# Kernel optimization log

Hardware: AMD Instinct MI355X
Metric: run time of the kernel (lower is better)

The kernel has to match this reference:

```python
import jax, jax.numpy as jnp
import numpy as np
import math

B, N, D = 64, 128, 128          # graphs, nodes per graph, d_model
D_STATE = 2                     # Mamba default d_state
D_CONV = 4                      # Mamba default conv kernel
DT_RANK = math.ceil(D / 16)     # 8
CUTOFF = 10.0
N_GAUSS = 50                    # GaussianSmearing(0, 10, 50)
EPS_RMS = 1e-5


def setup_inputs() -> dict:
    key = jax.random.key(0)
    ks = jax.random.split(key, 12)
    s = 0.05
    inp = {}
    inp['x'] = jax.random.normal(ks[0], (B * N, D), jnp.float32)
    inp['pos'] = jax.random.normal(ks[1], (B * N, 3), jnp.float32) * 5.0
    inp['map_idx'] = jax.random.randint(ks[2], (B * N,), 0, 16)
    inp['batch'] = jnp.repeat(jnp.arange(B), N)
    # RMSNorm
    inp['norm_w'] = jnp.ones((D,), jnp.float32)
    # simple message-passing gnn (stand-in for injected gnn module)
    inp['gnn_w1'] = jax.random.normal(ks[3], (D, D), jnp.float32) * s
    inp['gnn_b1'] = jnp.zeros((D,), jnp.float32)
    inp['gnn_w2'] = jax.random.normal(ks[4], (D, D), jnp.float32) * s
    inp['gnn_b2'] = jnp.zeros((D,), jnp.float32)
    # Linear(50, 1) on Gaussian-smeared edge distances
    inp['lin_w'] = jax.random.normal(ks[5], (N_GAUSS, 1), jnp.float32) * s
    inp['lin_b'] = jnp.zeros((1,), jnp.float32)
    # MambaBlock params (stored [in, out])
    inp['in_proj_w'] = jax.random.normal(ks[6], (D, 2 * D), jnp.float32) * s
    inp['conv_w'] = jax.random.normal(ks[7], (D, D_CONV), jnp.float32) * s
    inp['conv_b'] = jnp.zeros((D,), jnp.float32)
    inp['x_proj_w'] = jax.random.normal(ks[8], (D, DT_RANK + 2 * D_STATE), jnp.float32) * s
    inp['dt_proj_w'] = jax.random.normal(ks[9], (DT_RANK, D), jnp.float32) * s
    inp['dt_proj_b'] = jnp.zeros((D,), jnp.float32)
    inp['A_log'] = jnp.log(jnp.tile(jnp.arange(1, D_STATE + 1, dtype=jnp.float32), (D, 1)))
    inp['D_param'] = jnp.ones((D,), jnp.float32)
    inp['out_proj_w'] = jax.random.normal(ks[10], (D, D), jnp.float32) * s
    return inp


def _rmsnorm(x, w):
    return x * jax.lax.rsqrt(jnp.mean(x * x, axis=-1, keepdims=True) + EPS_RMS) * w


def _mamba(x_t, adj, in_proj_w, conv_w, conv_b, x_proj_w, dt_proj_w, dt_proj_b,
           A_log, D_param, out_proj_w):
    # x_t: [N, D] node sequence for one graph; adj: [N, N] dense edge-value matrix
    L = x_t.shape[0]
    A = -jnp.exp(A_log)                                   # [D, S]
    xr = x_t @ in_proj_w                                  # [L, 2D]
    xm, res = xr[:, :D], xr[:, D:]
    # causal depthwise conv1d (padding d_conv-1, truncated to L)
    xp = jnp.pad(xm, ((D_CONV - 1, 0), (0, 0)))
    xc = conv_b + sum(xp[j:j + L] * conv_w[:, j] for j in range(D_CONV))
    xc = jax.nn.silu(xc)                                  # [L, D]
    dbl = xc @ x_proj_w                                   # [L, dt_rank + 2S]
    delta = dbl[:, :DT_RANK]
    Bm = dbl[:, DT_RANK:DT_RANK + D_STATE]                # [L, S]
    Cm = dbl[:, DT_RANK + D_STATE:]                       # [L, S]
    delta = jax.nn.softplus(delta @ dt_proj_w + dt_proj_b)  # [L, D]
    # temp_adj_padded: ones [D, D] with adjacency slice in top-left
    m = min(L, D)
    adj_pad = jnp.ones((D, D), dtype=adj.dtype).at[:m, :m].set(adj[:m, :m])
    delta_p = delta @ adj_pad                             # [L, D]
    dA = jnp.exp(delta_p[:, :, None] * A[None])           # [L, D, S]
    dBu = delta_p[:, :, None] * Bm[:, None, :] * xc[:, :, None]

    def step(h, t):
        dA_t, dBu_t, C_t = t
        h = dA_t * h + dBu_t                              # [D, S]
        return h, h @ C_t                                 # [D]

    _, ys = jax.lax.scan(step, jnp.zeros((D, D_STATE), x_t.dtype), (dA, dBu, Cm))
    y = ys + xc * D_param
    y = y * jax.nn.silu(res)
    out = y @ out_proj_w
    return jnp.where(jnp.isfinite(out), out, 0.0)


def reference(x, pos, map_idx, batch, norm_w, gnn_w1, gnn_b1, gnn_w2, gnn_b2,
              lin_w, lin_b, in_proj_w, conv_w, conv_b, x_proj_w, dt_proj_w,
              dt_proj_b, A_log, D_param, out_proj_w):
    x1 = _rmsnorm(x, norm_w)                              # [B*N, D]
    xg = x1.reshape(B, N, D)
    pg = pos.reshape(B, N, 3)
    # per-graph radius graph (dense): dist + edge mask
    diff = pg[:, :, None, :] - pg[:, None, :, :]          # [B, N, N, 3]
    d2 = jnp.sum(diff * diff, axis=-1)
    eye = jnp.eye(N, dtype=bool)[None]
    dist = jnp.sqrt(jnp.where(eye, 1.0, d2))              # safe sqrt on diag
    edge_mask = (~eye) & (dist < CUTOFF)                  # [B, N, N]
    em = edge_mask.astype(x1.dtype)
    # simple message-passing gnn: mean-aggregate relu(Wx) over radius neighbors
    h = jax.nn.relu(xg @ gnn_w1 + gnn_b1)
    deg = jnp.clip(jnp.sum(em, axis=-1, keepdims=True), 1.0, None)
    agg = jnp.einsum('bij,bjd->bid', em, h) / deg
    x2 = agg @ gnn_w2 + gnn_b2                            # [B, N, D]
    # GaussianSmearing(0, 10, 50) + Linear(50, 1) -> dense edge-value matrix
    offsets = jnp.linspace(0.0, 10.0, N_GAUSS)
    coeff = -0.5 / (offsets[1] - offsets[0]) ** 2
    smear = jnp.exp(coeff * (dist[..., None] - offsets) ** 2)  # [B, N, N, 50]
    d_dense = smear @ lin_w[:, 0] + lin_b[0]
    adj = jnp.where(edge_mask, d_dense, 0.0)              # sparse-to-dense
    # Mamba mixer over each graph's node sequence
    mix = jax.vmap(lambda xt, a: _mamba(xt, a, in_proj_w, conv_w, conv_b,
                                        x_proj_w, dt_proj_w, dt_proj_b,
                                        A_log, D_param, out_proj_w))
    x3 = mix(x2, adj).reshape(B * N, D)
    output = x3 + x1
    return (output, pos, map_idx)
```

## Files before the change

### kernel.cpp

```cpp
#include <hip/hip_runtime.h>
#include <math.h>

#define B_ 64
#define N_ 128
#define D_ 128
#define BN_ 8192
#define NG_ 50
#define CUTOFF_ 10.0f

typedef __attribute__((ext_vector_type(8))) short short8v;
typedef __attribute__((ext_vector_type(4))) float f32x4;
#define MFMA16 __builtin_amdgcn_mfma_f32_16x16x32_bf16

__device__ __forceinline__ float bf2f(unsigned short h) {
    return __builtin_bit_cast(float, ((unsigned int)h) << 16);
}
__device__ __forceinline__ unsigned short f2bf(float f) {
    unsigned int u = __builtin_bit_cast(unsigned int, f);
    return (unsigned short)((u + 0x7FFFu + ((u >> 16) & 1u)) >> 16);
}
__device__ __forceinline__ void splitbf(float x, unsigned short& h, unsigned short& l) {
    h = f2bf(x);
    l = f2bf(x - bf2f(h));
}
__device__ __forceinline__ void gl_lds(const void* g, void* l) {
    __builtin_amdgcn_global_load_lds(
        (const __attribute__((address_space(1))) void*)g,
        (__attribute__((address_space(3))) void*)l, 16, 0, 0);
}

__global__ __launch_bounds__(256) void setup_k(
        const float* __restrict__ x, const float* __restrict__ norm_w,
        const float* __restrict__ pos, const int* __restrict__ mi,
        const float* __restrict__ lin_w, const float* __restrict__ lin_b,
        const float* __restrict__ w1, const float* __restrict__ w2,
        const float* __restrict__ b2, const float* __restrict__ in_proj,
        const float* __restrict__ xpw, const float* __restrict__ dtw,
        const float* __restrict__ out_proj,
        unsigned short* __restrict__ w1Th, unsigned short* __restrict__ w1Tl,
        unsigned short* __restrict__ WdTh, unsigned short* __restrict__ WdTl,
        unsigned short* __restrict__ opTh, unsigned short* __restrict__ opTl,
        unsigned short* __restrict__ WfTh, unsigned short* __restrict__ WfTl,
        float* __restrict__ bfv,
        float* __restrict__ x1f, unsigned short* __restrict__ x1h,
        unsigned short* __restrict__ x1l,
        unsigned short* __restrict__ adjh, unsigned short* __restrict__ adjl,
        unsigned short* __restrict__ emh, float* __restrict__ rdeg,
        float* __restrict__ out) {
    int blk = blockIdx.x, t = threadIdx.x;
    if (blk < 513) {
        if (blk < 128) {
            if (t < 128) {
                unsigned short h, l;
                splitbf(w1[blk * 128 + t], h, l);
                w1Th[t * 128 + blk] = h; w1Tl[t * 128 + blk] = l;
            }
        } else if (blk < 256) {
            int m = blk - 128;
            if (t < 128) {
                float s = 0.0f;
                #pragma unroll
                for (int r = 0; r < 8; r++) s = fmaf(xpw[m * 12 + r], dtw[r * 128 + t], s);
                unsigned short h, l; splitbf(s, h, l);
                WdTh[t * 128 + m] = h; WdTl[t * 128 + m] = l;
            }
        } else if (blk < 384) {
            int k = blk - 256;
            if (t < 128) {
                unsigned short h, l;
                splitbf(out_proj[k * 128 + t], h, l);
                opTh[t * 128 + k] = h; opTl[t * 128 + k] = l;
            }
        } else if (blk < 512) {
            int k = blk - 384;
            float s = 0.0f;
            #pragma unroll 8
            for (int j = 0; j < 128; j++) s = fmaf(w2[k * 128 + j], in_proj[j * 256 + t], s);
            unsigned short h, l; splitbf(s, h, l);
            WfTh[t * 128 + k] = h; WfTl[t * 128 + k] = l;
        } else {
            float s = 0.0f;
            #pragma unroll 8
            for (int j = 0; j < 128; j++) s = fmaf(b2[j], in_proj[j * 256 + t], s);
            bfv[t] = s;
        }
    } else if (blk < 642) {
        int idx = (blk - 513) * 256 + t;
        if (idx < BN_ * 3) out[(size_t)BN_ * D_ + idx] = pos[idx];
        if (idx < BN_) out[(size_t)BN_ * D_ + BN_ * 3 + idx] = (float)mi[idx];
    } else if (blk < 2690) {
        int rblk = blk - 642;
        int wv = t >> 6, ln = t & 63;
        int row = rblk * 4 + wv;
        const float2* xr = reinterpret_cast<const float2*>(x) + (size_t)row * 64;
        float2 v = xr[ln];
        float s = fmaf(v.x, v.x, v.y * v.y);
        #pragma unroll
        for (int o = 32; o > 0; o >>= 1) s += __shfl_down(s, o, 64);
        float tot = __shfl(s, 0, 64);
        float r = rsqrtf(tot * (1.0f / D_) + 1e-5f);
        float2 wv2 = reinterpret_cast<const float2*>(norm_w)[ln];
        float o0 = v.x * r * wv2.x, o1 = v.y * r * wv2.y;
        reinterpret_cast<float2*>(x1f)[(size_t)row * 64 + ln] = make_float2(o0, o1);
        unsigned short h0, l0, h1, l1;
        splitbf(o0, h0, l0); splitbf(o1, h1, l1);
        reinterpret_cast<ushort2*>(x1h)[(size_t)row * 64 + ln] = make_ushort2(h0, h1);
        reinterpret_cast<ushort2*>(x1l)[(size_t)row * 64 + ln] = make_ushort2(l0, l1);
    } else {
        __shared__ float px[N_], py[N_], pz[N_];
        __shared__ float lw[NG_];
        __shared__ int degs[8];
        int ablk = blk - 2690;
        int bx = ablk & 15, b = ablk >> 4;
        if (t < N_) {
            const float* p = pos + (size_t)(b * N_ + t) * 3;
            px[t] = p[0]; py[t] = p[1]; pz[t] = p[2];
        } else if (t - N_ < NG_) {
            lw[t - N_] = lin_w[t - N_];
        }
        if (t >= 248) degs[t - 248] = 0;
        __syncthreads();
        float linb = lin_b[0];
        int j = t & 127;
        int il = t >> 7;
        const float DEL = 10.0f / 49.0f;
        const float COEFF = -0.5f / (DEL * DEL);
        #pragma unroll
        for (int p = 0; p < 4; p++) {
            int i = bx * 8 + p * 2 + il;
            float dx = px[i] - px[j], dy = py[i] - py[j], dz = pz[i] - pz[j];
            float d2 = dx * dx + dy * dy + dz * dz;
            float dist = (i == j) ? 1.0f : sqrtf(d2);
            bool edge = (i != j) && (dist < CUTOFF_);
            float val = 0.0f;
            if (edge) {
                int g0 = (int)ceilf((dist - 1.75f) / DEL); if (g0 < 0) g0 = 0;
                int g1 = (int)floorf((dist + 1.75f) / DEL); if (g1 > NG_ - 1) g1 = NG_ - 1;
                float dm = dist - (float)g0 * DEL;
                float tg = expf(COEFF * dm * dm);
                float ug = expf(COEFF * DEL * (DEL - 2.0f * dm));
                float s = linb;
                for (int g = g0; g <= g1; g++) {
                    s = fmaf(lw[g], tg, s);
                    tg *= ug;
                    ug *= 0.36787944117144233f;
                }
                val = s;
            }
            size_t idx = ((size_t)b * N_ + i) * N_ + j;
            unsigned short h, l; splitbf(val, h, l);
            adjh[idx] = h; adjl[idx] = l;
            emh[idx] = edge ? 0x3F80 : 0;
            unsigned long long msk = __ballot(edge);
            if ((t & 63) == 0) atomicAdd(&degs[p * 2 + il], __popcll(msk));
        }
        __syncthreads();
        if (t < 8) {
            int dg = degs[t];
            rdeg[(size_t)b * N_ + bx * 8 + t] = 1.0f / (float)(dg > 0 ? dg : 1);
        }
    }
}

#define AHOFF 0
#define ALOFF 8192
#define BHOFF 16384
#define BLOFF 32768
template <int EPI, bool ALO>
__global__ __launch_bounds__(256, 3) void mgemm_k(
        const unsigned short* __restrict__ Ah, const unsigned short* __restrict__ Al,
        const unsigned short* __restrict__ BTh, const unsigned short* __restrict__ BTl,
        const float* __restrict__ bias, const float* __restrict__ AUX,
        float* __restrict__ Cf, unsigned short* __restrict__ Ch,
        unsigned short* __restrict__ Cl, int cstride, int wbs) {
    extern __shared__ char sm[];
    int tid = threadIdx.x;
    int row_base = blockIdx.x * 32;
    int col_base = blockIdx.y * 64;

    const unsigned short* pBh = BTh;
    const unsigned short* pBl = BTl;
    if (wbs) {
        size_t bo = (size_t)(row_base >> 7) * (size_t)wbs;
        pBh += bo; pBl += bo;
    }

    #pragma unroll
    for (int i = 0; i < 2; i++) {
        int s = tid + i * 256;
        int row = s >> 4, inner = s & 15;
        int gb = (inner * 16) ^ ((row & 7) << 4);
        size_t gsrc = (size_t)(row_base + row) * 256 + gb;
        gl_lds((const char*)Ah + gsrc, sm + AHOFF + s * 16);
        if (ALO) gl_lds((const char*)Al + gsrc, sm + ALOFF + s * 16);
    }
    #pragma unroll
    for (int i = 0; i < 4; i++) {
        int s = tid + i * 256;
        int n = s >> 4, inner = s & 15;
        int gb = (inner * 16) ^ ((n & 7) << 4);
        size_t gsrc = (size_t)(col_base + n) * 256 + gb;
        gl_lds((const char*)pBh + gsrc, sm + BHOFF + s * 16);
        gl_lds((const char*)pBl + gsrc, sm + BLOFF + s * 16);
    }
    __syncthreads();

    int w = tid >> 6, l = tid & 63;
    int rlow = l & 15, kb_lane = (l >> 4) * 16;
    int nB = w * 16 + rlow;
    int nswz = (nB & 7) << 4;
    f32x4 acc[2] = {{0.f, 0.f, 0.f, 0.f}, {0.f, 0.f, 0.f, 0.f}};
    #pragma unroll
    for (int kb = 0; kb < 4; kb++) {
        int kbyte = kb * 64 + kb_lane;
        short8v bh = *(const short8v*)(sm + BHOFF + nB * 256 + (kbyte ^ nswz));
        short8v bl = *(const short8v*)(sm + BLOFF + nB * 256 + (kbyte ^ nswz));
        #pragma unroll
        for (int rf = 0; rf < 2; rf++) {
            int ra = rf * 16 + rlow;
            int aswz = (ra & 7) << 4;
            short8v ah = *(const short8v*)(sm + AHOFF + ra * 256 + (kbyte ^ aswz));
            acc[rf] = MFMA16(ah, bh, acc[rf], 0, 0, 0);
            acc[rf] = MFMA16(ah, bl, acc[rf], 0, 0, 0);
            if (ALO) {
                short8v al_ = *(const short8v*)(sm + ALOFF + ra * 256 + (kbyte ^ aswz));
                acc[rf] = MFMA16(al_, bh, acc[rf], 0, 0, 0);
            }
        }
    }

    int colg = col_base + w * 16 + rlow;
    #pragma unroll
    for (int rf = 0; rf < 2; rf++) {
        int row0 = row_base + rf * 16 + (l >> 4) * 4;
        if (EPI == 1) {
            float b_ = bias[colg];
            unsigned short hh[4], ll[4];
            #pragma unroll
            for (int q = 0; q < 4; q++) {
                float t = fmaxf(acc[rf][q] + b_, 0.0f);
                splitbf(t, hh[q], ll[q]);
            }
            size_t bb = (size_t)(row0 >> 7) * 16384 + (size_t)colg * 128 + (row0 & 127);
            *reinterpret_cast<ushort4*>(Ch + bb) = make_ushort4(hh[0], hh[1], hh[2], hh[3]);
            *reinterpret_cast<ushort4*>(Cl + bb) = make_ushort4(ll[0], ll[1], ll[2], ll[3]);
        } else {
            #pragma unroll
            for (int q = 0; q < 4; q++) {
                int row = row0 + q;
                float t = acc[rf][q];
                if (EPI == 2) {
                    t *= AUX[row];
                    unsigned short h, lo; splitbf(t, h, lo);
                    Ch[(size_t)row * 128 + colg] = h;
                    Cl[(size_t)row * 128 + colg] = lo;
                }
                if (EPI == 5) {
                    t = isfinite(t) ? t : 0.0f;
                    t += AUX[(size_t)row * 128 + colg];
                    Cf[(size_t)row * cstride + colg] = t;
                }
            }
        }
    }
}

__device__ __forceinline__ void st128(char* dst, const char* g, int tid) {
    #pragma unroll
    for (int i = 0; i < 4; i++) {
        int s = tid + i * 512;
        int row = s >> 4, inner = s & 15;
        gl_lds(g + row * 256 + ((inner * 16) ^ ((row & 7) << 4)), dst + s * 16);
    }
}
__device__ __forceinline__ void stA48(char* dst, const char* g, int r0, int tid) {
    #pragma unroll
    for (int i = 0; i < 2; i++) {
        int s = tid + i * 512;
        if (s < 768) {
            int lr = s >> 4, inner = s & 15;
            int srow = r0 - 16 + lr; if (srow < 0) srow = 0;
            gl_lds(g + srow * 256 + ((inner * 16) ^ ((lr & 7) << 4)), dst + s * 16);
        }
    }
}
template <int NRF>
__device__ __forceinline__ void fpass(const char* sm, int ah, int al, int bh, int bl,
                                      int w, int l, f32x4 (&acc)[NRF]) {
    int rlow = l & 15, khi = (l >> 4) * 16;
    int nB = w * 16 + rlow;
    int nkey = (nB & 7) << 4;
    #pragma unroll
    for (int kb = 0; kb < 4; kb++) {
        int kbyte = kb * 64 + khi;
        short8v bhv = *(const short8v*)(sm + bh + nB * 256 + (kbyte ^ nkey));
        short8v blv = *(const short8v*)(sm + bl + nB * 256 + (kbyte ^ nkey));
        #pragma unroll
        for (int rf = 0; rf < NRF; rf++) {
            int ra = rf * 16 + rlow;
            int ao = ra * 256 + (kbyte ^ ((ra & 7) << 4));
            short8v ahv = *(const short8v*)(sm + ah + ao);
            short8v alv = *(const short8v*)(sm + al + ao);
            acc[rf] = MFMA16(ahv, bhv, acc[rf], 0, 0, 0);
            acc[rf] = MFMA16(ahv, blv, acc[rf], 0, 0, 0);
            acc[rf] = MFMA16(alv, bhv, acc[rf], 0, 0, 0);
        }
    }
}

__global__ __launch_bounds__(512, 2) void fused_k(
        const unsigned short* __restrict__ aggh, const unsigned short* __restrict__ aggl,
        const unsigned short* __restrict__ WfTh, const unsigned short* __restrict__ WfTl,
        const float* __restrict__ bfv,
        const float* __restrict__ conv_w, const float* __restrict__ conv_b,
        const float* __restrict__ xpw,
        const unsigned short* __restrict__ WdTh, const unsigned short* __restrict__ WdTl,
        const float* __restrict__ dtb,
        const unsigned short* __restrict__ adjh, const unsigned short* __restrict__ adjl,
        float* __restrict__ resT, float* __restrict__ xcT,
        float* __restrict__ bcT, float* __restrict__ dpT) {
    __shared__ __align__(16) char sm[163840];
    const int AH = 0, AL = 12288, XM = 24576, BH = 49152, BL = 81920,
              XCH = 114688, XCL = 122880, DH = 131072, DL = 139264, XCF = 147456;
    int blk = blockIdx.x, tid = threadIdx.x;
    int b = blk >> 2, r0 = (blk & 3) * 32;
    int w = tid >> 6, l = tid & 63;
    int rlow = l & 15, qrow = (l >> 4) * 4;

    stA48(sm + AH, (const char*)aggh + (size_t)b * 32768, r0, tid);
    stA48(sm + AL, (const char*)aggl + (size_t)b * 32768, r0, tid);
    st128(sm + BH, (const char*)WfTh, tid);
    st128(sm + BL, (const char*)WfTl, tid);
    __syncthreads();

    f32x4 acc[3] = {{0.f,0.f,0.f,0.f},{0.f,0.f,0.f,0.f},{0.f,0.f,0.f,0.f}};
    fpass<3>(sm, AH, AL, BH, BL, w, l, acc);
    __syncthreads();
    st128(sm + BH, (const char*)WfTh + 32768, tid);
    st128(sm + BL, (const char*)WfTl + 32768, tid);
    {
        int colg = w * 16 + rlow;
        float bb = bfv[colg];
        #pragma unroll
        for (int rf = 0; rf < 3; rf++) {
            #pragma unroll
            for (int q = 0; q < 4; q++) {
                int lr = rf * 16 + qrow + q;
                *(float*)(sm + XM + lr * 512 + ((colg * 4) ^ ((lr & 7) << 4))) =
                    acc[rf][q] + bb;
            }
        }
    }
    __syncthreads();

    f32x4 acc2[3] = {{0.f,0.f,0.f,0.f},{0.f,0.f,0.f,0.f},{0.f,0.f,0.f,0.f}};
    fpass<3>(sm, AH, AL, BH, BL, w, l, acc2);
    {
        int colg = w * 16 + rlow;
        float bb = bfv[128 + colg];
        #pragma unroll
        for (int rf = 1; rf < 3; rf++) {
            int lr0 = rf * 16 + qrow;
            int tt = r0 + lr0 - 16;
            float v[4];
            #pragma unroll
            for (int q = 0; q < 4; q++) {
                float rs = acc2[rf][q] + bb;
                v[q] = rs / (1.0f + expf(-rs));
            }
            *reinterpret_cast<float4*>(resT + ((size_t)b * 128 + colg) * 128 + tt) =
                make_float4(v[0], v[1], v[2], v[3]);
        }
    }
    __syncthreads();

    st128(sm + BH, (const char*)WdTh, tid);
    st128(sm + BL, (const char*)WdTl, tid);
    {
        int ot = tid >> 4, dg = tid & 15;
        float pc0 = 0, pc1 = 0, pc2 = 0, pc3 = 0;
        #pragma unroll
        for (int k = 0; k < 8; k++) {
            int d = dg * 8 + k;
            float accv = conv_b[d];
            #pragma unroll
            for (int jj = 0; jj < 4; jj++) {
                int tt = r0 + ot + jj - 3;
                if (tt >= 0) {
                    int lr = ot + jj - 3 + 16;
                    float xv = *(const float*)(sm + XM + lr * 512 +
                                               ((d * 4) ^ ((lr & 7) << 4)));
                    accv = fmaf(xv, conv_w[d * 4 + jj], accv);
                }
            }
            float xc = accv / (1.0f + expf(-accv));
            unsigned short hh, ll; splitbf(xc, hh, ll);
            int pb = ot * 256 + ((d * 2) ^ ((ot & 7) << 4));
            *(unsigned short*)(sm + XCH + pb) = hh;
            *(unsigned short*)(sm + XCL + pb) = ll;
            *(float*)(sm + XCF + ot * 512 + ((d * 4) ^ ((ot & 7) << 4))) = xc;
            float4 xw = *(const float4*)(xpw + d * 12 + 8);
            pc0 = fmaf(xc, xw.x, pc0); pc1 = fmaf(xc, xw.y, pc1);
            pc2 = fmaf(xc, xw.z, pc2); pc3 = fmaf(xc, xw.w, pc3);
        }
        #pragma unroll
        for (int m = 1; m < 16; m <<= 1) {
            pc0 += __shfl_xor(pc0, m, 64);
            pc1 += __shfl_xor(pc1, m, 64);
            pc2 += __shfl_xor(pc2, m, 64);
            pc3 += __shfl_xor(pc3, m, 64);
        }
        if (dg < 4) {
            float pv = dg == 0 ? pc0 : dg == 1 ? pc1 : dg == 2 ? pc2 : pc3;
            bcT[(size_t)b * 512 + dg * 128 + r0 + ot] = pv;
        }
    }
    __syncthreads();

    {
        int d = tid & 127, tg = tid >> 7;
        float v[8];
        #pragma unroll
        for (int k = 0; k < 8; k++) {
            int ot = tg * 8 + k;
            v[k] = *(const float*)(sm + XCF + ot * 512 + ((d * 4) ^ ((ot & 7) << 4)));
        }
        float* dst = xcT + ((size_t)b * 128 + d) * 128 + r0 + tg * 8;
        *reinterpret_cast<float4*>(dst) = make_float4(v[0], v[1], v[2], v[3]);
        *reinterpret_cast<float4*>(dst + 4) = make_float4(v[4], v[5], v[6], v[7]);
    }

    f32x4 dacc[2] = {{0.f,0.f,0.f,0.f},{0.f,0.f,0.f,0.f}};
    fpass<2>(sm, XCH, XCL, BH, BL, w, l, dacc);
    {
        int colg = w * 16 + rlow;
        float db = dtb[colg];
        #pragma unroll
        for (int rf = 0; rf < 2; rf++) {
            #pragma unroll
            for (int q = 0; q < 4; q++) {
                int lr = rf * 16 + qrow + q;
                float t = dacc[rf][q] + db;
                t = fmaxf(t, 0.0f) + log1pf(expf(-fabsf(t)));
                unsigned short hh, ll; splitbf(t, hh, ll);
                int pb = lr * 256 + ((colg * 2) ^ ((lr & 7) << 4));
                *(unsigned short*)(sm + DH + pb) = hh;
                *(unsigned short*)(sm + DL + pb) = ll;
            }
        }
    }
    __syncthreads();

    st128(sm + BH, (const char*)adjh + (size_t)b * 32768, tid);
    st128(sm + BL, (const char*)adjl + (size_t)b * 32768, tid);
    __syncthreads();
    f32x4 pacc[2] = {{0.f,0.f,0.f,0.f},{0.f,0.f,0.f,0.f}};
    fpass<2>(sm, DH, DL, BH, BL, w, l, pacc);
    {
        int colg = w * 16 + rlow;
        #pragma unroll
        for (int rf = 0; rf < 2; rf++) {
            int lr0 = rf * 16 + qrow;
            *reinterpret_cast<float4*>(dpT + ((size_t)b * 128 + colg) * 128 + r0 + lr0) =
                make_float4(pacc[rf][0], pacc[rf][1], pacc[rf][2], pacc[rf][3]);
        }
    }
}

__global__ __launch_bounds__(256) void scan_k(const float* __restrict__ dpT,
                                              const float* __restrict__ xcT,
                                              const float* __restrict__ bcT,
                                              const float* __restrict__ resT,
                                              const float* __restrict__ A_log,
                                              const float* __restrict__ Dpar,
                                              unsigned short* __restrict__ yh,
                                              unsigned short* __restrict__ yl) {
    __shared__ float lds[3 * 4096 + 512];
    float* bcl = lds + 12288;
    int b = blockIdx.x;
    int t = threadIdx.x;
    if (t < 128) {
        float4 v = reinterpret_cast<const float4*>(bcT + (size_t)b * 512)[t];
        *reinterpret_cast<float4*>(bcl + t * 4) = v;
    }
    float a1 = 0.f, a2 = 0.f, Dp = 0.f;
    if (t < 128) {
        a1 = -expf(A_log[t * 2]);
        a2 = -expf(A_log[t * 2 + 1]);
        Dp = Dpar[t];
    }
    float h1 = 0.0f, h2 = 0.0f;
    const float4* dp4 = reinterpret_cast<const float4*>(dpT + (size_t)b * 16384);
    const float4* xc4 = reinterpret_cast<const float4*>(xcT + (size_t)b * 16384);
    const float4* rr4 = reinterpret_cast<const float4*>(resT + (size_t)b * 16384);
    size_t ybase = (size_t)b * 16384 + t;
    for (int c = 0; c < 4; c++) {
        __syncthreads();
        #pragma unroll
        for (int k = 0; k < 4; k++) {
            int q = t + k * 256;
            int dd = q >> 3, tq = q & 7;
            int gidx = dd * 32 + c * 8 + tq;
            float4 vd = dp4[gidx], vx = xc4[gidx], vr = rr4[gidx];
            #pragma unroll
            for (int j = 0; j < 4; j++) {
                int tp = tq * 4 + j;
                int sw = dd ^ tp;
                float fd = (j == 0) ? vd.x : (j == 1) ? vd.y : (j == 2) ? vd.z : vd.w;
                float fx = (j == 0) ? vx.x : (j == 1) ? vx.y : (j == 2) ? vx.z : vx.w;
                float fr = (j == 0) ? vr.x : (j == 1) ? vr.y : (j == 2) ? vr.z : vr.w;
                lds[tp * 128 + sw] = fd;
                lds[4096 + tp * 128 + sw] = fx;
                lds[8192 + tp * 128 + sw] = fr;
            }
        }
        __syncthreads();
        if (t < 128) {
            #pragma unroll 8
            for (int tp = 0; tp < 32; tp++) {
                int sw = t ^ tp;
                float dpv = lds[tp * 128 + sw];
                float xcv = lds[4096 + tp * 128 + sw];
                float rv  = lds[8192 + tp * 128 + sw];
                int tg = c * 32 + tp;
                float bm0 = bcl[tg], bm1 = bcl[128 + tg];
                float cm0 = bcl[256 + tg], cm1 = bcl[384 + tg];
                float e1 = expf(dpv * a1), e2 = expf(dpv * a2);
                float bu = dpv * xcv;
                h1 = fmaf(e1, h1, bu * bm0);
                h2 = fmaf(e2, h2, bu * bm1);
                float y = fmaf(h1, cm0, h2 * cm1);
                float yv = fmaf(xcv, Dp, y) * rv;
                unsigned short hh, ll; splitbf(yv, hh, ll);
                yh[ybase + (size_t)tg * 128] = hh;
                yl[ybase + (size_t)tg * 128] = ll;
            }
        }
    }
}

extern "C" void kernel_launch(void* const* d_in, const int* in_sizes, int n_in,
                              void* d_out, int out_size, void* d_ws, size_t ws_size,
                              hipStream_t stream) {
    const float* x        = (const float*)d_in[0];
    const float* pos      = (const float*)d_in[1];
    const int*   mi       = (const int*)d_in[2];
    const float* norm_w   = (const float*)d_in[4];
    const float* w1       = (const float*)d_in[5];
    const float* b1       = (const float*)d_in[6];
    const float* w2       = (const float*)d_in[7];
    const float* b2       = (const float*)d_in[8];
    const float* lin_w    = (const float*)d_in[9];
    const float* lin_b    = (const float*)d_in[10];
    const float* in_proj  = (const float*)d_in[11];
    const float* conv_w   = (const float*)d_in[12];
    const float* conv_b   = (const float*)d_in[13];
    const float* xpw      = (const float*)d_in[14];
    const float* dtw      = (const float*)d_in[15];
    const float* dtb      = (const float*)d_in[16];
    const float* A_log    = (const float*)d_in[17];
    const float* Dpar     = (const float*)d_in[18];
    const float* out_proj = (const float*)d_in[19];

    float* out = (float*)d_out;
    char* base = (char*)d_ws;
    const size_t MB = 1u << 20;
    const size_t PL = 1048576;

    float* x1f  = (float*)(base);
    float* resT = (float*)(base + 8 * MB);
    float* dpT  = (float*)(base + 12 * MB);
    float* xcT  = (float*)(base + 16 * MB);
    float* bcT  = (float*)(base + 20 * MB);
    float* rdeg = (float*)(base + 20 * MB + 131072);

    unsigned short* P = (unsigned short*)(base + 21 * MB);
    unsigned short* x1h  = P +  0 * PL;
    unsigned short* x1l  = P +  1 * PL;
    unsigned short* hTh  = P +  2 * PL;
    unsigned short* hTl  = P +  3 * PL;
    unsigned short* aggh = P +  4 * PL;
    unsigned short* aggl = P +  5 * PL;
    unsigned short* xch  = P +  6 * PL;
    unsigned short* xcl  = P +  7 * PL;
    unsigned short* dlh  = P +  8 * PL;
    unsigned short* dll  = P +  9 * PL;
    unsigned short* yh   = P + 10 * PL;
    unsigned short* yl   = P + 11 * PL;
    unsigned short* adjh = P + 12 * PL;
    unsigned short* adjl = P + 13 * PL;
    unsigned short* emh  = P + 14 * PL;

    unsigned short* W = (unsigned short*)(base + 52 * MB);
    unsigned short* w1Th = W;
    unsigned short* w1Tl = W + 16384;
    unsigned short* WdTh = W + 2 * 16384;
    unsigned short* WdTl = W + 3 * 16384;
    unsigned short* opTh = W + 4 * 16384;
    unsigned short* opTl = W + 5 * 16384;
    unsigned short* WfTh = W + 6 * 16384;
    unsigned short* WfTl = WfTh + 32768;
    float* bfv = (float*)(WfTl + 32768);

    const size_t gsm = 49152;

    setup_k<<<3714, 256, 0, stream>>>(x, norm_w, pos, mi, lin_w, lin_b,
                                      w1, w2, b2, in_proj, xpw, dtw, out_proj,
                                      w1Th, w1Tl, WdTh, WdTl, opTh, opTl, WfTh, WfTl,
                                      bfv, x1f, x1h, x1l, adjh, adjl, emh, rdeg, out);
    mgemm_k<1, true><<<dim3(256, 2), 256, gsm, stream>>>(
        x1h, x1l, w1Th, w1Tl, b1, nullptr, nullptr, hTh, hTl, 128, 0);
    mgemm_k<2, false><<<dim3(256, 2), 256, gsm, stream>>>(
        emh, emh, hTh, hTl, nullptr, rdeg, nullptr, aggh, aggl, 128, 16384);
    fused_k<<<256, 512, 0, stream>>>(aggh, aggl, WfTh, WfTl, bfv,
                                     conv_w, conv_b, xpw, WdTh, WdTl, dtb,
                                     adjh, adjl, resT, xcT, bcT, dpT);
    scan_k<<<B_, 256, 0, stream>>>(dpT, xcT, bcT, resT, A_log, Dpar, yh, yl);
    mgemm_k<5, true><<<dim3(256, 2), 256, gsm, stream>>>(
        yh, yl, opTh, opTl, nullptr, x1f, out, nullptr, nullptr, 128, 0);
}
```

Baseline: 86.91 us.

## Fuse selective scan with output projection GEMM and residual add

Merges the scan kernel and the final out_proj GEMM into one kernel per graph. The scan now writes its bf16 hi/lo y values into swizzled LDS instead of global memory, then the same block loads the out_proj weights and runs split-bf16 MFMA to produce out = y@W + x1. This removes one kernel launch and the y round trip through global memory. In exchange the output GEMM runs on only 64 blocks with about 114KB of LDS each, which lowers parallelism compared with the earlier 512-block GEMM.

```diff
diff --git a/kernel.cpp b/kernel.cpp
--- a/kernel.cpp
+++ b/kernel.cpp
@@ -467,16 +467,16 @@
     }
 }
 
-__global__ __launch_bounds__(256) void scan_k(const float* __restrict__ dpT,
-                                              const float* __restrict__ xcT,
-                                              const float* __restrict__ bcT,
-                                              const float* __restrict__ resT,
-                                              const float* __restrict__ A_log,
-                                              const float* __restrict__ Dpar,
-                                              unsigned short* __restrict__ yh,
-                                              unsigned short* __restrict__ yl) {
-    __shared__ float lds[3 * 4096 + 512];
-    float* bcl = lds + 12288;
+__global__ __launch_bounds__(256) void scanout_k(
+        const float* __restrict__ dpT, const float* __restrict__ xcT,
+        const float* __restrict__ bcT, const float* __restrict__ resT,
+        const float* __restrict__ A_log, const float* __restrict__ Dpar,
+        const unsigned short* __restrict__ opTh, const unsigned short* __restrict__ opTl,
+        const float* __restrict__ x1f, float* __restrict__ out) {
+    __shared__ __align__(16) char smb[116736];
+    float* lds = (float*)smb;
+    float* bcl = (float*)(smb + 49152);
+    const int YH = 51200, YL = 83968;
     int b = blockIdx.x;
     int t = threadIdx.x;
     if (t < 128) {
@@ -493,7 +493,6 @@
     const float4* dp4 = reinterpret_cast<const float4*>(dpT + (size_t)b * 16384);
     const float4* xc4 = reinterpret_cast<const float4*>(xcT + (size_t)b * 16384);
     const float4* rr4 = reinterpret_cast<const float4*>(resT + (size_t)b * 16384);
-    size_t ybase = (size_t)b * 16384 + t;
     for (int c = 0; c < 4; c++) {
         __syncthreads();
         #pragma unroll
@@ -532,10 +531,62 @@
                 float y = fmaf(h1, cm0, h2 * cm1);
                 float yv = fmaf(xcv, Dp, y) * rv;
                 unsigned short hh, ll; splitbf(yv, hh, ll);
-                yh[ybase + (size_t)tg * 128] = hh;
-                yl[ybase + (size_t)tg * 128] = ll;
-            }
-        }
+                int byo = (t * 2) ^ ((tg & 7) << 4);
+                *(unsigned short*)(smb + YH + tg * 256 + byo) = hh;
+                *(unsigned short*)(smb + YL + tg * 256 + byo) = ll;
+            }
+        }
+    }
+    __syncthreads();
+
+    int w = t >> 6, l = t & 63;
+    int rlow = l & 15, kb_lane = (l >> 4) * 16;
+    int nB = w * 16 + rlow;
+    int nswz = (nB & 7) << 4;
+    for (int cu = 0; cu < 2; cu++) {
+        #pragma unroll
+        for (int i = 0; i < 4; i++) {
+            int s = t + i * 256;
+            int row = s >> 4, inner = s & 15;
+            int gb = (inner * 16) ^ ((row & 7) << 4);
+            size_t gsrc = (size_t)(cu * 64 + row) * 256 + gb;
+            gl_lds((const char*)opTh + gsrc, smb + s * 16);
+            gl_lds((const char*)opTl + gsrc, smb + 16384 + s * 16);
+        }
+        __syncthreads();
+        int colg = cu * 64 + nB;
+        for (int ru = 0; ru < 4; ru++) {
+            f32x4 acc[2] = {{0.f, 0.f, 0.f, 0.f}, {0.f, 0.f, 0.f, 0.f}};
+            #pragma unroll
+            for (int kb = 0; kb < 4; kb++) {
+                int kbyte = kb * 64 + kb_lane;
+                short8v bh = *(const short8v*)(smb + nB * 256 + (kbyte ^ nswz));
+                short8v bl = *(const short8v*)(smb + 16384 + nB * 256 + (kbyte ^ nswz));
+                #pragma unroll
+                for (int rf = 0; rf < 2; rf++) {
+                    int ra = ru * 32 + rf * 16 + rlow;
+                    int aswz = (ra & 7) << 4;
+                    short8v ah = *(const short8v*)(smb + YH + ra * 256 + (kbyte ^ aswz));
+                    acc[rf] = MFMA16(ah, bh, acc[rf], 0, 0, 0);
+                    acc[rf] = MFMA16(ah, bl, acc[rf], 0, 0, 0);
+                    short8v al_ = *(const short8v*)(smb + YL + ra * 256 + (kbyte ^ aswz));
+                    acc[rf] = MFMA16(al_, bh, acc[rf], 0, 0, 0);
+                }
+            }
+            #pragma unroll
+            for (int rf = 0; rf < 2; rf++) {
+                int row0 = ru * 32 + rf * 16 + (l >> 4) * 4;
+                #pragma unroll
+                for (int q = 0; q < 4; q++) {
+                    int row = row0 + q;
+                    float tv = acc[rf][q];
+                    tv = isfinite(tv) ? tv : 0.0f;
+                    size_t g = (size_t)(b * 128 + row) * 128 + colg;
+                    out[g] = tv + x1f[g];
+                }
+            }
+        }
+        __syncthreads();
     }
 }
 
@@ -585,8 +636,6 @@
     unsigned short* xcl  = P +  7 * PL;
     unsigned short* dlh  = P +  8 * PL;
     unsigned short* dll  = P +  9 * PL;
-    unsigned short* yh   = P + 10 * PL;
-    unsigned short* yl   = P + 11 * PL;
     unsigned short* adjh = P + 12 * PL;
     unsigned short* adjl = P + 13 * PL;
     unsigned short* emh  = P + 14 * PL;
@@ -615,7 +664,6 @@
     fused_k<<<256, 512, 0, stream>>>(aggh, aggl, WfTh, WfTl, bfv,
                                      conv_w, conv_b, xpw, WdTh, WdTl, dtb,
                                      adjh, adjl, resT, xcT, bcT, dpT);
-    scan_k<<<B_, 256, 0, stream>>>(dpT, xcT, bcT, resT, A_log, Dpar, yh, yl);
-    mgemm_k<5, true><<<dim3(256, 2), 256, gsm, stream>>>(
-        yh, yl, opTh, opTl, nullptr, x1f, out, nullptr, nullptr, 128, 0);
-}
+    scanout_k<<<B_, 256, 0, stream>>>(dpT, xcT, bcT, resT, A_log, Dpar,
+                                      opTh, opTl, x1f, out);
+}
```

Measured after the change: 83.64 us (median of 2 runs). 3.8% less time.
